# Optimization experiments

Hardware: AMD Instinct MI355X
Metric: run time of the kernel (lower is better)

Reference implementation:

```python
import jax, jax.numpy as jnp
import numpy as np

B, S, D = 2, 2048, 1024
H = 16
HD = D // H  # 64


def setup_inputs() -> dict:
    key = jax.random.key(0)
    ks = jax.random.split(key, 9)
    s = 1.0 / np.sqrt(D)
    x = jax.random.normal(ks[0], (B, S, D), dtype=jnp.float32)
    Wq = jax.random.normal(ks[1], (D, D), dtype=jnp.float32) * s
    Wk = jax.random.normal(ks[2], (D, D), dtype=jnp.float32) * s
    Wv = jax.random.normal(ks[3], (D, D), dtype=jnp.float32) * s
    Wo = jax.random.normal(ks[4], (D, D), dtype=jnp.float32) * s
    bq = jnp.zeros((D,), jnp.float32)
    bk = jnp.zeros((D,), jnp.float32)
    bv = jnp.zeros((D,), jnp.float32)
    bo = jnp.zeros((D,), jnp.float32)
    # causal mask, broadcastable to (B, H, S, S)
    mask = jnp.tril(jnp.ones((S, S), dtype=bool))[None, None, :, :]
    return {"x": x, "Wq": Wq, "bq": bq, "Wk": Wk, "bk": bk,
            "Wv": Wv, "bv": bv, "Wo": Wo, "bo": bo, "mask": mask}


def _split_heads(t):
    # (B, S, D) -> (B, H, S, HD)
    b, s, _ = t.shape
    return t.reshape(b, s, H, HD).transpose(0, 2, 1, 3)


def reference(x, Wq, bq, Wk, bk, Wv, bv, Wo, bo, mask):
    q = _split_heads(x @ Wq + bq)
    k = _split_heads(x @ Wk + bk)
    v = _split_heads(x @ Wv + bv)
    scale = 1.0 / jnp.sqrt(jnp.asarray(HD, dtype=q.dtype))
    scores = jnp.einsum('bhqd,bhkd->bhqk', q, k) * scale
    large_neg = jnp.finfo(scores.dtype).min
    scores = jnp.where(mask, scores, large_neg)
    attn = jax.nn.softmax(scores, axis=-1)
    out = jnp.einsum('bhqk,bhkd->bhqd', attn, v)  # (B,H,S,HD)
    out = out.transpose(0, 2, 1, 3).reshape(x.shape[0], x.shape[1], D)
    return out @ Wo + bo
```

## Files before the change

kernel.cpp:

```cpp
#include <hip/hip_runtime.h>
#include <hip/hip_bf16.h>

typedef __attribute__((ext_vector_type(8))) short bf16x8;
typedef __attribute__((ext_vector_type(4))) float f32x4;
typedef __attribute__((ext_vector_type(16))) float f32x16;

#define B_DIM  2
#define S_DIM  2048
#define D_DIM  1024
#define H_DIM  16
#define HD_DIM 64

__device__ __forceinline__ float bf2f(ushort u) {
    union { unsigned int ui; float f; } c; c.ui = ((unsigned int)u) << 16; return c.f;
}
__device__ __forceinline__ ushort f2bf(float f) {
    __hip_bfloat16 h = __float2bfloat16(f);
    return *reinterpret_cast<ushort*>(&h);
}

__device__ __forceinline__ void async_cp16(const ushort* g, ushort* l) {
    __builtin_amdgcn_global_load_lds(
        (const __attribute__((address_space(1))) void*)g,
        (__attribute__((address_space(3))) void*)l, 16, 0, 0);
}

__device__ __forceinline__ unsigned int cvt_pk_bf16(float lo, float hi) {
    unsigned int d;
    asm volatile("v_cvt_pk_bf16_f32 %0, %1, %2" : "=v"(d) : "v"(lo), "v"(hi));
    return d;
}
__device__ __forceinline__ void pl32swap(unsigned int& a, unsigned int& b) {
    asm volatile("v_permlane32_swap_b32 %0, %1" : "+v"(a), "+v"(b));
}

__global__ __launch_bounds__(256) void detect_kernel(const ushort* __restrict__ x,
                                                     int* __restrict__ flag) {
    __shared__ int any;
    int tid = threadIdx.x;
    if (tid == 0) any = 0;
    __syncthreads();
    int cnt = 0;
    for (int j = 0; j < 64; ++j) {
        ushort u = x[tid * 64 + j];
        if (((u >> 7) & 0xFF) == 0xFF) cnt++;
    }
    if (cnt) atomicOr(&any, 1);
    __syncthreads();
    if (tid == 0) *flag = any ? 1 : 0;
}

__global__ __launch_bounds__(256) void prep_kernel(const void* __restrict__ x,
                                                   const void* __restrict__ Wq,
                                                   const void* __restrict__ Wk,
                                                   const void* __restrict__ Wv,
                                                   const void* __restrict__ Wo,
                                                   const void* __restrict__ bq,
                                                   const void* __restrict__ bk,
                                                   const void* __restrict__ bv,
                                                   const void* __restrict__ bo,
                                                   ushort* __restrict__ xc,
                                                   ushort* __restrict__ Wqkvt,
                                                   ushort* __restrict__ Wot,
                                                   float* __restrict__ biasf,
                                                   const int* __restrict__ flag) {
    int tid = threadIdx.x;
    int z = blockIdx.z;
    bool isf32 = (*flag != 0);

    if (z == 4) {
        int t = (blockIdx.y * 16 + blockIdx.x) * 256 + tid;
#pragma unroll
        for (int c = 0; c < 8; ++c) {
            int i = t + c * 65536;
            if (isf32) {
                const float* s = (const float*)x;
                f32x4 a = *(const f32x4*)&s[(size_t)i * 8];
                f32x4 b = *(const f32x4*)&s[(size_t)i * 8 + 4];
                bf16x8 o;
                o[0] = f2bf(a.x); o[1] = f2bf(a.y); o[2] = f2bf(a.z); o[3] = f2bf(a.w);
                o[4] = f2bf(b.x); o[5] = f2bf(b.y); o[6] = f2bf(b.z); o[7] = f2bf(b.w);
                *(bf16x8*)&xc[(size_t)i * 8] = o;
            } else {
                *(bf16x8*)&xc[(size_t)i * 8] =
                    *(const bf16x8*)&((const ushort*)x)[(size_t)i * 8];
            }
        }
        return;
    }
    if (z == 5) {
        int bid = blockIdx.y * 16 + blockIdx.x;
        if (bid >= 16) return;
        int i = bid * 256 + tid;
        int w = i >> 10, j = i & 1023;
        const void* s = (w == 0) ? bq : (w == 1) ? bk : (w == 2) ? bv : bo;
        biasf[i] = isf32 ? ((const float*)s)[j] : bf2f(((const ushort*)s)[j]);
        return;
    }

    __shared__ ushort tile[64][72];
    const void* src = (z == 0) ? Wq : (z == 1) ? Wk : (z == 2) ? Wv : Wo;
    ushort* dst = (z < 3) ? (Wqkvt + (size_t)z * D_DIM * D_DIM) : Wot;
    int r0 = blockIdx.y * 64, c0 = blockIdx.x * 64;
#pragma unroll
    for (int p = 0; p < 2; ++p) {
        int r = p * 32 + (tid >> 3);
        int c = (tid & 7) * 8;
        if (isf32) {
            const float* s = (const float*)src;
            f32x4 a = *(const f32x4*)&s[(size_t)(r0 + r) * D_DIM + c0 + c];
            f32x4 b = *(const f32x4*)&s[(size_t)(r0 + r) * D_DIM + c0 + c + 4];
            tile[r][c + 0] = f2bf(a.x); tile[r][c + 1] = f2bf(a.y);
            tile[r][c + 2] = f2bf(a.z); tile[r][c + 3] = f2bf(a.w);
            tile[r][c + 4] = f2bf(b.x); tile[r][c + 5] = f2bf(b.y);
            tile[r][c + 6] = f2bf(b.z); tile[r][c + 7] = f2bf(b.w);
        } else {
            *(bf16x8*)&tile[r][c] =
                *(const bf16x8*)&((const ushort*)src)[(size_t)(r0 + r) * D_DIM + c0 + c];
        }
    }
    __syncthreads();
#pragma unroll
    for (int p = 0; p < 2; ++p) {
        int n  = p * 32 + (tid >> 3);
        int cc = (tid & 7) * 8;
        bf16x8 v;
#pragma unroll
        for (int e = 0; e < 8; ++e) v[e] = (short)tile[cc + e][n];
        *(bf16x8*)&dst[(size_t)(c0 + n) * D_DIM + r0 + cc] = v;
    }
}

__global__ __launch_bounds__(256) void gemm128_kernel(const ushort* __restrict__ A,
                                                      const ushort* __restrict__ Bt,
                                                      const float* __restrict__ bias,
                                                      ushort* __restrict__ qkout,
                                                      ushort* __restrict__ vtout) {
    __shared__ ushort As[128 * 64];
    __shared__ ushort Bs[128 * 64];
    int tid  = threadIdx.x;
    int wave = tid >> 6;
    int lane = tid & 63;
    int l16  = lane & 15;
    int quad = lane >> 4;
    int m0   = blockIdx.y * 128;
    int n0   = blockIdx.x * 128;
    int wm   = wave >> 1;
    int wn   = wave & 1;
    const int K = 1024;

    f32x4 acc[4][4];
#pragma unroll
    for (int i = 0; i < 4; ++i)
#pragma unroll
        for (int j = 0; j < 4; ++j) acc[i][j] = (f32x4){0.f, 0.f, 0.f, 0.f};

    int lrow = lane >> 3;
    int gcol = ((lane & 7) ^ lrow) * 8;
    int sw   = l16 & 7;

    for (int kt = 0; kt < 16; ++kt) {
        int k0 = kt * 64;
#pragma unroll
        for (int j = 0; j < 4; ++j) {
            int chunk = wave * 4 + j;
            int grow  = chunk * 8 + lrow;
            async_cp16(&A[(size_t)(m0 + grow) * K + k0 + gcol], &As[chunk * 512]);
            async_cp16(&Bt[(size_t)(n0 + grow) * K + k0 + gcol], &Bs[chunk * 512]);
        }
        __syncthreads();

#pragma unroll
        for (int kb = 0; kb < 2; ++kb) {
            bf16x8 af[4], bf[4];
#pragma unroll
            for (int i = 0; i < 4; ++i)
                af[i] = *(const bf16x8*)&As[(wm * 64 + i * 16 + l16) * 64 +
                                            (((kb * 4 + quad) ^ sw) << 3)];
#pragma unroll
            for (int j = 0; j < 4; ++j)
                bf[j] = *(const bf16x8*)&Bs[(wn * 64 + j * 16 + l16) * 64 +
                                            (((kb * 4 + quad) ^ sw) << 3)];
#pragma unroll
            for (int i = 0; i < 4; ++i)
#pragma unroll
                for (int j = 0; j < 4; ++j)
                    acc[i][j] = __builtin_amdgcn_mfma_f32_16x16x32_bf16(af[i], bf[j],
                                                                        acc[i][j], 0, 0, 0);
        }
        __syncthreads();
    }

    const size_t TSZ = (size_t)B_DIM * H_DIM * S_DIM * HD_DIM;
#pragma unroll
    for (int j = 0; j < 4; ++j) {
        int n = n0 + wn * 64 + j * 16 + l16;
        float bv = bias[n];
        int which = n >> 10;
        int n1 = n & 1023;
        int h = n1 >> 6, hd = n1 & 63;
#pragma unroll
        for (int i = 0; i < 4; ++i) {
            int mb = m0 + wm * 64 + i * 16 + quad * 4;
            int b = mb >> 11, s = mb & (S_DIM - 1);
            float v4[4];
#pragma unroll
            for (int r = 0; r < 4; ++r) v4[r] = acc[i][j][r] + bv;
            if (which == 2) {
                ushort pk[4];
#pragma unroll
                for (int r = 0; r < 4; ++r) pk[r] = f2bf(v4[r]);
                *(uint2*)&vtout[(((size_t)(b * H_DIM + h) * HD_DIM + hd)) * S_DIM + s] =
                    *(uint2*)pk;
            } else {
#pragma unroll
                for (int r = 0; r < 4; ++r) {
                    float v = v4[r];
                    if (which == 0) v *= 0.18033688011f;
                    qkout[which * TSZ +
                          ((((size_t)(b * H_DIM + h)) * S_DIM + s + r) << 6) + hd] = f2bf(v);
                }
            }
        }
    }
}

__global__ __launch_bounds__(256) void gemm64_kernel(const ushort* __restrict__ A,
                                                     const ushort* __restrict__ Bt,
                                                     const float* __restrict__ bias,
                                                     void* __restrict__ out,
                                                     const int* __restrict__ flag) {
    __shared__ ushort As[64 * 64];
    __shared__ ushort Bs[128 * 64];
    int tid  = threadIdx.x;
    int wave = tid >> 6;
    int lane = tid & 63;
    int l16  = lane & 15;
    int quad = lane >> 4;
    int m0   = blockIdx.y * 64;
    int n0   = blockIdx.x * 128;
    const int K = 1024;

    f32x4 acc[4][2];
#pragma unroll
    for (int i = 0; i < 4; ++i)
#pragma unroll
        for (int j = 0; j < 2; ++j) acc[i][j] = (f32x4){0.f, 0.f, 0.f, 0.f};

    int lrow = lane >> 3;
    int gcol = ((lane & 7) ^ lrow) * 8;
    int sw   = l16 & 7;

    for (int kt = 0; kt < 16; ++kt) {
        int k0 = kt * 64;
#pragma unroll
        for (int j = 0; j < 2; ++j) {
            int chunk = wave * 2 + j;
            int grow  = chunk * 8 + lrow;
            async_cp16(&A[(size_t)(m0 + grow) * K + k0 + gcol], &As[chunk * 512]);
        }
#pragma unroll
        for (int j = 0; j < 4; ++j) {
            int chunk = wave * 4 + j;
            int grow  = chunk * 8 + lrow;
            async_cp16(&Bt[(size_t)(n0 + grow) * K + k0 + gcol], &Bs[chunk * 512]);
        }
        __syncthreads();

#pragma unroll
        for (int kb = 0; kb < 2; ++kb) {
            bf16x8 af[4], bf[2];
#pragma unroll
            for (int i = 0; i < 4; ++i)
                af[i] = *(const bf16x8*)&As[(i * 16 + l16) * 64 +
                                            (((kb * 4 + quad) ^ sw) << 3)];
#pragma unroll
            for (int j = 0; j < 2; ++j)
                bf[j] = *(const bf16x8*)&Bs[(wave * 32 + j * 16 + l16) * 64 +
                                            (((kb * 4 + quad) ^ sw) << 3)];
#pragma unroll
            for (int i = 0; i < 4; ++i)
#pragma unroll
                for (int j = 0; j < 2; ++j)
                    acc[i][j] = __builtin_amdgcn_mfma_f32_16x16x32_bf16(af[i], bf[j],
                                                                        acc[i][j], 0, 0, 0);
        }
        __syncthreads();
    }

    int outf32 = *flag;
#pragma unroll
    for (int j = 0; j < 2; ++j) {
        int n = n0 + wave * 32 + j * 16 + l16;
        float bv = bias[n];
#pragma unroll
        for (int i = 0; i < 4; ++i)
#pragma unroll
            for (int r = 0; r < 4; ++r) {
                int m = m0 + i * 16 + quad * 4 + r;
                float v = acc[i][j][r] + bv;
                if (outf32) ((float*)out)[(size_t)m * D_DIM + n] = v;
                else        ((ushort*)out)[(size_t)m * D_DIM + n] = f2bf(v);
            }
    }
}

__global__ __launch_bounds__(256, 2) void attn_kernel(const ushort* __restrict__ Qg,
                                                      const ushort* __restrict__ Kg,
                                                      const ushort* __restrict__ Vt,
                                                      ushort* __restrict__ attn_out) {
    __shared__ ushort Ks[2][64 * 64];
    __shared__ ushort Vs[2][64 * 64];
    int tid  = threadIdx.x;
    int wave = tid >> 6;
    int lane = tid & 63;
    int l31  = lane & 31;
    int hi   = lane >> 5;
    int sw7  = lane & 7;
    int bh   = blockIdx.x;
    int y    = blockIdx.y;
    int qt   = (y < 8) ? y : (23 - y);
    int q0   = qt * 128;

    const ushort* Qb = Qg + (size_t)bh * S_DIM * HD_DIM;
    const ushort* Kb = Kg + (size_t)bh * S_DIM * HD_DIM;
    const ushort* Vb = Vt + (size_t)bh * HD_DIM * S_DIM;

    bf16x8 qf[4];
#pragma unroll
    for (int kk = 0; kk < 4; ++kk)
        qf[kk] = *(const bf16x8*)&Qb[(size_t)(q0 + wave * 32 + l31) * HD_DIM +
                                     kk * 16 + hi * 8];

    f32x16 o[2];
#pragma unroll
    for (int n = 0; n < 2; ++n)
#pragma unroll
        for (int r = 0; r < 16; ++r) o[n][r] = 0.f;
    float rsum = 0.f;

    int lrow = lane >> 3;
    int gcol = ((lane & 7) ^ lrow) * 8;

#pragma unroll
    for (int j = 0; j < 2; ++j) {
        int chunk = wave * 2 + j;
        int grow  = chunk * 8 + lrow;
        async_cp16(&Kb[(size_t)grow * HD_DIM + gcol], &Ks[0][chunk * 512]);
        async_cp16(&Vb[(size_t)grow * S_DIM + gcol], &Vs[0][chunk * 512]);
    }

    int ntiles = 2 * qt + 2;
    int p = 0;
    for (int t = 0; t < ntiles; ++t) {
        __syncthreads();
        if (t + 1 < ntiles) {
            int k1 = (t + 1) * 64;
#pragma unroll
            for (int j = 0; j < 2; ++j) {
                int chunk = wave * 2 + j;
                int grow  = chunk * 8 + lrow;
                async_cp16(&Kb[(size_t)(k1 + grow) * HD_DIM + gcol],
                           &Ks[p ^ 1][chunk * 512]);
                async_cp16(&Vb[(size_t)grow * S_DIM + k1 + gcol],
                           &Vs[p ^ 1][chunk * 512]);
            }
        }

        if (!(t == ntiles - 1 && wave < 2)) {
            int k0 = t * 64;

            f32x16 sc[2];
#pragma unroll
            for (int n = 0; n < 2; ++n)
#pragma unroll
                for (int r = 0; r < 16; ++r) sc[n][r] = 0.f;
            __builtin_amdgcn_s_setprio(1);
#pragma unroll
            for (int j = 0; j < 4; ++j)
#pragma unroll
                for (int mb = 0; mb < 2; ++mb) {
                    bf16x8 kf = *(const bf16x8*)&Ks[p][(mb * 32 + l31) * 64 +
                                                       (((2 * j + hi) ^ sw7) << 3)];
                    sc[mb] = __builtin_amdgcn_mfma_f32_32x32x16_bf16(kf, qf[j],
                                                                     sc[mb], 0, 0, 0);
                }
            __builtin_amdgcn_s_setprio(0);

            bf16x8 vf[4][2];
#pragma unroll
            for (int j = 0; j < 4; ++j)
#pragma unroll
                for (int nb = 0; nb < 2; ++nb)
                    vf[j][nb] = *(const bf16x8*)&Vs[p][(nb * 32 + l31) * 64 +
                                                       (((2 * j + hi) ^ sw7) << 3)];

            if (t == ntiles - 2 + (wave >> 1)) {
                int qglob = q0 + wave * 32 + l31;
#pragma unroll
                for (int mb = 0; mb < 2; ++mb)
#pragma unroll
                    for (int r = 0; r < 16; ++r) {
                        int key = k0 + mb * 32 + (r & 3) + 8 * (r >> 2) + 4 * hi;
                        if (key > qglob) sc[mb][r] = -1e30f;
                    }
            }

            bf16x8 pf[4];
#pragma unroll
            for (int mb = 0; mb < 2; ++mb) {
                unsigned int W[8];
#pragma unroll
                for (int g = 0; g < 4; ++g) {
                    float e0 = __builtin_amdgcn_exp2f(sc[mb][4 * g + 0]);
                    float e1 = __builtin_amdgcn_exp2f(sc[mb][4 * g + 1]);
                    float e2 = __builtin_amdgcn_exp2f(sc[mb][4 * g + 2]);
                    float e3 = __builtin_amdgcn_exp2f(sc[mb][4 * g + 3]);
                    rsum += (e0 + e1) + (e2 + e3);
                    W[2 * g]     = cvt_pk_bf16(e0, e1);
                    W[2 * g + 1] = cvt_pk_bf16(e2, e3);
                }
                pl32swap(W[0], W[2]); pl32swap(W[1], W[3]);
                pl32swap(W[4], W[6]); pl32swap(W[5], W[7]);
                union { unsigned int u[4]; bf16x8 v; } c0, c1;
                c0.u[0] = W[0]; c0.u[1] = W[1]; c0.u[2] = W[2]; c0.u[3] = W[3];
                c1.u[0] = W[4]; c1.u[1] = W[5]; c1.u[2] = W[6]; c1.u[3] = W[7];
                pf[2 * mb]     = c0.v;
                pf[2 * mb + 1] = c1.v;
            }

            __builtin_amdgcn_s_setprio(1);
#pragma unroll
            for (int j = 0; j < 4; ++j)
#pragma unroll
                for (int nb = 0; nb < 2; ++nb)
                    o[nb] = __builtin_amdgcn_mfma_f32_32x32x16_bf16(pf[j], vf[j][nb],
                                                                    o[nb], 0, 0, 0);
            __builtin_amdgcn_s_setprio(0);
        }
        p ^= 1;
    }

    rsum += __shfl_xor(rsum, 32, 64);
    float inv = 1.f / rsum;

    int b = bh >> 4, h = bh & 15;
#pragma unroll
    for (int nb = 0; nb < 2; ++nb)
#pragma unroll
        for (int r = 0; r < 16; ++r) {
            int qrow = (r & 3) + 8 * (r >> 2) + 4 * hi;
            float iv = __shfl(inv, qrow, 64);
            int q = q0 + wave * 32 + qrow;
            attn_out[(size_t)(b * S_DIM + q) * D_DIM + h * HD_DIM + nb * 32 + l31] =
                f2bf(o[nb][r] * iv);
        }
}

extern "C" void kernel_launch(void* const* d_in, const int* in_sizes, int n_in,
                              void* d_out, int out_size, void* d_ws, size_t ws_size,
                              hipStream_t stream) {
    const void* x  = d_in[0];
    const void* Wq = d_in[1];
    const void* bq = d_in[2];
    const void* Wk = d_in[3];
    const void* bk = d_in[4];
    const void* Wv = d_in[5];
    const void* bv = d_in[6];
    const void* Wo = d_in[7];
    const void* bo = d_in[8];

    char* ws = (char*)d_ws;
    const size_t MB = 1024 * 1024;
    const size_t base = 64 * 1024;
    int*    flag   = (int*)ws;
    float*  biasf  = (float*)(ws + 4096);
    ushort* xc     = (ushort*)(ws + base);
    ushort* Wqkvt  = (ushort*)(ws + base + 8  * MB);
    ushort* Wot    = (ushort*)(ws + base + 14 * MB);
    ushort* Qc     = (ushort*)(ws + base + 16 * MB);
    ushort* Vtp    = (ushort*)(ws + base + 40 * MB);
    ushort* attn   = xc;

    dim3 tb(256);

    detect_kernel<<<1, tb, 0, stream>>>((const ushort*)x, flag);

    dim3 pg(16, 16, 6);
    prep_kernel<<<pg, tb, 0, stream>>>(x, Wq, Wk, Wv, Wo, bq, bk, bv, bo,
                                       xc, Wqkvt, Wot, biasf, flag);

    dim3 gq(3 * D_DIM / 128, (B_DIM * S_DIM) / 128);
    gemm128_kernel<<<gq, tb, 0, stream>>>(xc, Wqkvt, biasf, Qc, Vtp);

    dim3 ag(B_DIM * H_DIM, S_DIM / 128);
    attn_kernel<<<ag, tb, 0, stream>>>(Qc, Qc + (size_t)B_DIM * H_DIM * S_DIM * HD_DIM,
                                       Vtp, attn);

    dim3 go(D_DIM / 128, (B_DIM * S_DIM) / 64);
    gemm64_kernel<<<go, tb, 0, stream>>>(attn, Wot, biasf + 3072, d_out, flag);
}
```

Before: 194.8 us.

## Split attention key range across two blocks and combine partials in new kernel

Each query tile's key tiles are split into two halves, each handled by a separate block that writes unnormalized fp32 partial outputs and row sums. A new combine kernel adds the two partials, normalizes, and writes bf16 for the output projection. This doubles the attention grid and evens out the causal work per block (launch bounds raised to 4), at the cost of extra fp32 global traffic (two 16MB partial buffers) and one more kernel launch. It relies on the existing fixed-max (no running max) softmax so that partials can be summed directly.

```diff
diff --git a/kernel.cpp b/kernel.cpp
--- a/kernel.cpp
+++ b/kernel.cpp
@@ -305,10 +305,12 @@
     }
 }
 
-__global__ __launch_bounds__(256, 2) void attn_kernel(const ushort* __restrict__ Qg,
+__global__ __launch_bounds__(256, 4) void attn_kernel(const ushort* __restrict__ Qg,
                                                       const ushort* __restrict__ Kg,
                                                       const ushort* __restrict__ Vt,
-                                                      ushort* __restrict__ attn_out) {
+                                                      float* __restrict__ pO0,
+                                                      float* __restrict__ pO1,
+                                                      float* __restrict__ Rsum) {
     __shared__ ushort Ks[2][64 * 64];
     __shared__ ushort Vs[2][64 * 64];
     int tid  = threadIdx.x;
@@ -319,7 +321,11 @@
     int sw7  = lane & 7;
     int bh   = blockIdx.x;
     int y    = blockIdx.y;
-    int qt   = (y < 8) ? y : (23 - y);
+    int qt   = 15 - (y >> 1);
+    int half = y & 1;
+    int nt2  = qt + 1;
+    int t_lo = half * nt2;
+    int t_hi = t_lo + nt2;
     int q0   = qt * 128;
 
     const ushort* Qb = Qg + (size_t)bh * S_DIM * HD_DIM;
@@ -341,20 +347,23 @@
 
     int lrow = lane >> 3;
     int gcol = ((lane & 7) ^ lrow) * 8;
-
-#pragma unroll
-    for (int j = 0; j < 2; ++j) {
-        int chunk = wave * 2 + j;
-        int grow  = chunk * 8 + lrow;
-        async_cp16(&Kb[(size_t)grow * HD_DIM + gcol], &Ks[0][chunk * 512]);
-        async_cp16(&Vb[(size_t)grow * S_DIM + gcol], &Vs[0][chunk * 512]);
-    }
-
-    int ntiles = 2 * qt + 2;
+    int qmin = q0 + wave * 32;
+
+    {
+        int kst = t_lo * 64;
+#pragma unroll
+        for (int j = 0; j < 2; ++j) {
+            int chunk = wave * 2 + j;
+            int grow  = chunk * 8 + lrow;
+            async_cp16(&Kb[(size_t)(kst + grow) * HD_DIM + gcol], &Ks[0][chunk * 512]);
+            async_cp16(&Vb[(size_t)grow * S_DIM + kst + gcol], &Vs[0][chunk * 512]);
+        }
+    }
+
     int p = 0;
-    for (int t = 0; t < ntiles; ++t) {
+    for (int t = t_lo; t < t_hi; ++t) {
         __syncthreads();
-        if (t + 1 < ntiles) {
+        if (t + 1 < t_hi) {
             int k1 = (t + 1) * 64;
 #pragma unroll
             for (int j = 0; j < 2; ++j) {
@@ -366,10 +375,9 @@
                            &Vs[p ^ 1][chunk * 512]);
             }
         }
-
-        if (!(t == ntiles - 1 && wave < 2)) {
-            int k0 = t * 64;
-
+        int k0 = t * 64;
+
+        if (k0 <= qmin + 31) {
             f32x16 sc[2];
 #pragma unroll
             for (int n = 0; n < 2; ++n)
@@ -395,8 +403,8 @@
                     vf[j][nb] = *(const bf16x8*)&Vs[p][(nb * 32 + l31) * 64 +
                                                        (((2 * j + hi) ^ sw7) << 3)];
 
-            if (t == ntiles - 2 + (wave >> 1)) {
-                int qglob = q0 + wave * 32 + l31;
+            if (k0 + 63 > qmin) {
+                int qglob = qmin + l31;
 #pragma unroll
                 for (int mb = 0; mb < 2; ++mb)
 #pragma unroll
@@ -442,19 +450,44 @@
     }
 
     rsum += __shfl_xor(rsum, 32, 64);
-    float inv = 1.f / rsum;
-
+
+    float* pO = half ? pO1 : pO0;
     int b = bh >> 4, h = bh & 15;
 #pragma unroll
     for (int nb = 0; nb < 2; ++nb)
 #pragma unroll
         for (int r = 0; r < 16; ++r) {
             int qrow = (r & 3) + 8 * (r >> 2) + 4 * hi;
-            float iv = __shfl(inv, qrow, 64);
             int q = q0 + wave * 32 + qrow;
-            attn_out[(size_t)(b * S_DIM + q) * D_DIM + h * HD_DIM + nb * 32 + l31] =
-                f2bf(o[nb][r] * iv);
-        }
+            pO[(size_t)(b * S_DIM + q) * D_DIM + h * HD_DIM + nb * 32 + l31] = o[nb][r];
+        }
+    if (lane < 32)
+        Rsum[half * (32 * S_DIM) + bh * S_DIM + qmin + lane] = rsum;
+}
+
+__global__ __launch_bounds__(256) void combine_kernel(const float* __restrict__ pO0,
+                                                      const float* __restrict__ pO1,
+                                                      const float* __restrict__ Rsum,
+                                                      ushort* __restrict__ attn) {
+    int e8 = blockIdx.x * 256 + threadIdx.x;
+    int d8 = e8 & 127;
+    int s  = (e8 >> 7) & (S_DIM - 1);
+    int b  = e8 >> 18;
+    int bh = b * H_DIM + (d8 >> 3);
+    float r0 = Rsum[bh * S_DIM + s];
+    float r1 = Rsum[32 * S_DIM + bh * S_DIM + s];
+    float inv = 1.f / (r0 + r1);
+    size_t base = (size_t)e8 * 8;
+    f32x4 a0 = *(const f32x4*)&pO0[base];
+    f32x4 a1 = *(const f32x4*)&pO0[base + 4];
+    f32x4 c0 = *(const f32x4*)&pO1[base];
+    f32x4 c1 = *(const f32x4*)&pO1[base + 4];
+    bf16x8 ov;
+    ov[0] = f2bf((a0.x + c0.x) * inv); ov[1] = f2bf((a0.y + c0.y) * inv);
+    ov[2] = f2bf((a0.z + c0.z) * inv); ov[3] = f2bf((a0.w + c0.w) * inv);
+    ov[4] = f2bf((a1.x + c1.x) * inv); ov[5] = f2bf((a1.y + c1.y) * inv);
+    ov[6] = f2bf((a1.z + c1.z) * inv); ov[7] = f2bf((a1.w + c1.w) * inv);
+    *(bf16x8*)&attn[base] = ov;
 }
 
 extern "C" void kernel_launch(void* const* d_in, const int* in_sizes, int n_in,
@@ -480,6 +513,9 @@
     ushort* Wot    = (ushort*)(ws + base + 14 * MB);
     ushort* Qc     = (ushort*)(ws + base + 16 * MB);
     ushort* Vtp    = (ushort*)(ws + base + 40 * MB);
+    float*  pO0    = (float*)(ws + base + 48 * MB);
+    float*  pO1    = (float*)(ws + base + 64 * MB);
+    float*  Rsum   = (float*)(ws + base + 80 * MB);
     ushort* attn   = xc;
 
     dim3 tb(256);
@@ -493,9 +529,11 @@
     dim3 gq(3 * D_DIM / 128, (B_DIM * S_DIM) / 128);
     gemm128_kernel<<<gq, tb, 0, stream>>>(xc, Wqkvt, biasf, Qc, Vtp);
 
-    dim3 ag(B_DIM * H_DIM, S_DIM / 128);
+    dim3 ag(B_DIM * H_DIM, 32);
     attn_kernel<<<ag, tb, 0, stream>>>(Qc, Qc + (size_t)B_DIM * H_DIM * S_DIM * HD_DIM,
-                                       Vtp, attn);
+                                       Vtp, pO0, pO1, Rsum);
+
+    combine_kernel<<<2048, tb, 0, stream>>>(pO0, pO1, Rsum, attn);
 
     dim3 go(D_DIM / 128, (B_DIM * S_DIM) / 64);
     gemm64_kernel<<<go, tb, 0, stream>>>(attn, Wot, biasf + 3072, d_out, flag);
```

Result: slower. 202.3 us (+3.9%).
